# Kernel optimization log

Measured on AMD Instinct MI355X. Metric: run time of the kernel, lower is better.

The kernel has to match this reference:

```python
import jax, jax.numpy as jnp
import numpy as np

WS = 16         # window size
NH = 16         # num heads
EPS = 1e-6


def _ln(x):
    m = jnp.mean(x, axis=-1, keepdims=True)
    v = jnp.var(x, axis=-1, keepdims=True)
    return (x - m) * jax.lax.rsqrt(v + EPS)


def _modulate(x, shift, scale):
    return x * (1.0 + scale[:, None, :]) + shift[:, None, :]


def setup_inputs() -> dict:
    key = jax.random.key(0)
    ks = jax.random.split(key, 14)
    D, HD = 1024, 64
    s = 0.02
    return {
        'x': jax.random.normal(ks[0], (4, 4096, D), jnp.float32),
        'c': jax.random.normal(ks[1], (4, D), jnp.float32),
        'qkv_w': jax.random.normal(ks[2], (3 * D, D), jnp.float32) * s,
        'qkv_b': jax.random.normal(ks[3], (3 * D,), jnp.float32) * s,
        'proj_w': jax.random.normal(ks[4], (D, D), jnp.float32) * s,
        'proj_b': jax.random.normal(ks[5], (D,), jnp.float32) * s,
        'rel_pos_h': jax.random.normal(ks[6], (2 * WS - 1, HD), jnp.float32) * s,
        'rel_pos_w': jax.random.normal(ks[7], (2 * WS - 1, HD), jnp.float32) * s,
        'adaLN_w': jax.random.normal(ks[8], (6 * D, D), jnp.float32) * s,
        'adaLN_b': jax.random.normal(ks[9], (6 * D,), jnp.float32) * s,
        'fc1_w': jax.random.normal(ks[10], (4 * D, D), jnp.float32) * s,
        'fc1_b': jax.random.normal(ks[11], (4 * D,), jnp.float32) * s,
        'fc2_w': jax.random.normal(ks[12], (D, 4 * D), jnp.float32) * s,
        'fc2_b': jax.random.normal(ks[13], (D,), jnp.float32) * s,
    }


def _window_attention(x, qkv_w, qkv_b, proj_w, proj_b, rel_pos_h, rel_pos_w):
    # x: [N, T, D] with T = h*w, h = w = sqrt(T)
    N, T, D = x.shape
    h = w = int(round(T ** 0.5))
    nwh, nww = h // WS, w // WS  # grid divides evenly -> no padding
    hd = D // NH
    scale = hd ** -0.5

    # window partition: [N, h, w, D] -> [B, WS, WS, D], B = N*nwh*nww
    xw = x.reshape(N, nwh, WS, nww, WS, D).transpose(0, 1, 3, 2, 4, 5)
    xw = xw.reshape(N * nwh * nww, WS, WS, D)
    B = xw.shape[0]
    L = WS * WS

    qkv = (xw.reshape(B, L, D) @ qkv_w.T + qkv_b)  # [B, L, 3D]
    qkv = qkv.reshape(B, L, 3, NH, hd).transpose(2, 0, 3, 1, 4)  # [3, B, NH, L, hd]
    qkv = qkv.reshape(3, B * NH, L, hd)
    q, k, v = qkv[0], qkv[1], qkv[2]

    attn = jnp.einsum('bqc,bkc->bqk', q * scale, k)  # [B*NH, L, L]

    # decomposed relative position bias (q_size == k_size == WS)
    coords = jnp.arange(WS)
    rel_idx = coords[:, None] - coords[None, :] + (WS - 1)  # [WS, WS]
    Rh = rel_pos_h[rel_idx]  # [WS(q_h), WS(k_h), hd]
    Rw = rel_pos_w[rel_idx]  # [WS(q_w), WS(k_w), hd]
    rq = q.reshape(B * NH, WS, WS, hd)
    rel_h = jnp.einsum('bhwc,hkc->bhwk', rq, Rh)  # [B*NH, WS, WS, WS(kh)]
    rel_w = jnp.einsum('bhwc,wkc->bhwk', rq, Rw)  # [B*NH, WS, WS, WS(kw)]
    attn = (attn.reshape(B * NH, WS, WS, WS, WS)
            + rel_h[:, :, :, :, None]
            + rel_w[:, :, :, None, :]).reshape(B * NH, L, L)

    probs = jax.nn.softmax(attn, axis=-1)
    out = probs @ v  # [B*NH, L, hd]
    out = out.reshape(B, NH, WS, WS, hd).transpose(0, 2, 3, 1, 4).reshape(B, WS, WS, D)
    out = out @ proj_w.T + proj_b

    # window unpartition: [B, WS, WS, D] -> [N, T, D]
    out = out.reshape(N, nwh, nww, WS, WS, D).transpose(0, 1, 3, 2, 4, 5)
    return out.reshape(N, T, D)


def reference(x, c, qkv_w, qkv_b, proj_w, proj_b, rel_pos_h, rel_pos_w,
              adaLN_w, adaLN_b, fc1_w, fc1_b, fc2_w, fc2_b):
    D = x.shape[-1]
    mod = jax.nn.silu(c) @ adaLN_w.T + adaLN_b  # [N, 6D]
    sh_msa, sc_msa, g_msa, sh_mlp, sc_mlp, g_mlp = jnp.split(mod, 6, axis=1)

    a_in = _modulate(_ln(x), sh_msa, sc_msa)
    a_out = _window_attention(a_in, qkv_w, qkv_b, proj_w, proj_b, rel_pos_h, rel_pos_w)
    x = x + g_msa[:, None, :] * a_out

    m_in = _modulate(_ln(x), sh_mlp, sc_mlp)
    hdn = jax.nn.gelu(m_in @ fc1_w.T + fc1_b, approximate=True)
    m_out = hdn @ fc2_w.T + fc2_b
    x = x + g_mlp[:, None, :] * m_out
    return x
```

## Files before the change

kernel.cpp:

```cpp
#include <hip/hip_runtime.h>
#include <cstdint>
#include <cstddef>


typedef float  f32x4    __attribute__((ext_vector_type(4)));
typedef __bf16 bf16x8_t __attribute__((ext_vector_type(8)));
typedef __bf16 bf16x4_t __attribute__((ext_vector_type(4)));

#define DEV __device__ __forceinline__

DEV void gload_lds16(const void* g, void* l) {
    auto gp = (const uint32_t __attribute__((address_space(1)))*)(uintptr_t)g;
    auto lp = (uint32_t __attribute__((address_space(3)))*)(uint32_t)(uintptr_t)l;
    __builtin_amdgcn_global_load_lds(gp, lp, 16, 0, 0);
}

DEV bf16x8_t lds_frag(const __bf16* base, int row, int chunk, int row_elems) {
    return *(const bf16x8_t*)(base + row * row_elems + ((chunk ^ (row & 7)) << 3));
}

DEV bf16x8_t p_frag(const __bf16* base, int row, int chunk) {
    return *(const bf16x8_t*)(base + row * 32 + ((chunk ^ ((row >> 1) & 3)) << 3));
}

DEV int vt_addr(int d, int k) {
    return d * 64 + ((((k >> 3) ^ (d & 7) ^ ((d >> 3) & 7)) << 3) | (k & 7));
}

DEV float gelu_tanh(float v) {
    float u = 0.7978845608028654f * (v + 0.044715f * v * v * v);
    float e = __expf(2.f * u);
    float th = 1.f - 2.f / (e + 1.f);
    return 0.5f * v * (1.f + th);
}

DEV int win2tok(int r) {
    int nb = r >> 12, wi = (r >> 8) & 15, l = r & 255;
    return (nb << 12) + (wi >> 2) * 1024 + (l >> 4) * 64 + (wi & 3) * 16 + (l & 15);
}

__global__ void silu_k(const float* __restrict__ c, float* __restrict__ o, int n) {
    int i = blockIdx.x * 256 + threadIdx.x;
    if (i < n) { float v = c[i]; o[i] = v / (1.f + __expf(-v)); }
}

__global__ void zero_k(float* o, int n) {
    int i = blockIdx.x * 256 + threadIdx.x;
    if (i < n) o[i] = 0.f;
}

__global__ void conv_bf16(const float* __restrict__ s, __bf16* __restrict__ d, int n4) {
    int i = blockIdx.x * 256 + threadIdx.x;
    if (i < n4) {
        float4 v = ((const float4*)s)[i];
        bf16x4_t o; o[0] = (__bf16)v.x; o[1] = (__bf16)v.y; o[2] = (__bf16)v.z; o[3] = (__bf16)v.w;
        ((bf16x4_t*)d)[i] = o;
    }
}

__global__ __launch_bounds__(256)
void mod_gemv(const float* __restrict__ sc, const float* __restrict__ w,
              const float* __restrict__ b, float* __restrict__ mod) {
    int o = (blockIdx.x << 2) + (threadIdx.x >> 6);
    int lane = threadIdx.x & 63;
    int n = o / 6144, col = o % 6144;
    const float4* wr = (const float4*)(w + (size_t)col * 1024);
    const float4* sr = (const float4*)(sc + n * 1024);
    float acc = 0.f;
    #pragma unroll 4
    for (int i = lane; i < 256; i += 64) {
        float4 a = wr[i], x = sr[i];
        acc += a.x * x.x + a.y * x.y + a.z * x.z + a.w * x.w;
    }
    #pragma unroll
    for (int m = 1; m < 64; m <<= 1) acc += __shfl_xor(acc, m);
    if (lane == 0) mod[o] = acc + b[col];
}

__global__ __launch_bounds__(256)
void ln_mod_k(const float* __restrict__ src, const float* __restrict__ mod,
              int sh_off, int sc_off, __bf16* __restrict__ out, int permute, int r0) {
    int rl = blockIdx.x;
    int r = rl + r0;
    int nb = r >> 12;
    int t = permute ? win2tok(r) : r;
    float4 v = ((const float4*)(src + (size_t)t * 1024))[threadIdx.x];
    float s  = v.x + v.y + v.z + v.w;
    float sq = v.x * v.x + v.y * v.y + v.z * v.z + v.w * v.w;
    #pragma unroll
    for (int m = 1; m < 64; m <<= 1) { s += __shfl_xor(s, m); sq += __shfl_xor(sq, m); }
    __shared__ float ps[4], pq[4];
    int wv = threadIdx.x >> 6, ln = threadIdx.x & 63;
    if (ln == 0) { ps[wv] = s; pq[wv] = sq; }
    __syncthreads();
    s  = ps[0] + ps[1] + ps[2] + ps[3];
    sq = pq[0] + pq[1] + pq[2] + pq[3];
    float mean = s * (1.f / 1024.f);
    float var  = sq * (1.f / 1024.f) - mean * mean;
    float rstd = rsqrtf(var + 1e-6f);
    int c = threadIdx.x << 2;
    const float* mrow = mod + nb * 6144;
    float4 scv = *(const float4*)(mrow + sc_off + c);
    float4 shv = *(const float4*)(mrow + sh_off + c);
    bf16x4_t o;
    o[0] = (__bf16)((v.x - mean) * rstd * (1.f + scv.x) + shv.x);
    o[1] = (__bf16)((v.y - mean) * rstd * (1.f + scv.y) + shv.y);
    o[2] = (__bf16)((v.z - mean) * rstd * (1.f + scv.z) + shv.z);
    o[3] = (__bf16)((v.w - mean) * rstd * (1.f + scv.w) + shv.w);
    *(bf16x4_t*)(out + (size_t)rl * 1024 + c) = o;
}

template <int PM, int PN>
DEV void mfma16(f32x4 (&acc)[8][4], bf16x8_t (&fa)[4][2], bf16x8_t (&fb)[2][2][2]) {
    #pragma unroll
    for (int ks = 0; ks < 2; ++ks)
        #pragma unroll
        for (int mi = 0; mi < 4; ++mi)
            #pragma unroll
            for (int nn = 0; nn < 2; ++nn)
                acc[PM * 4 + mi][PN * 2 + nn] = __builtin_amdgcn_mfma_f32_16x16x32_bf16(
                    fa[mi][ks], fb[PN][nn][ks], acc[PM * 4 + mi][PN * 2 + nn], 0, 0, 0);
}

#define GBAR  __builtin_amdgcn_s_barrier()
#define VM6   asm volatile("s_waitcnt vmcnt(6)" ::: "memory")
#define PRIO1 __builtin_amdgcn_s_setprio(1)
#define PRIO0 __builtin_amdgcn_s_setprio(0)

template <int EPI>
__global__ __launch_bounds__(512)
void gemm256(const __bf16* __restrict__ A, const __bf16* __restrict__ B,
             const float* __restrict__ bias, void* __restrict__ Cout,
             const float* __restrict__ extra, const float* __restrict__ mod,
             int N, int K, int r0, int gx) {
    extern __shared__ __align__(16) char smem[];
    __bf16* lA = (__bf16*)smem;
    __bf16* lB = lA + 2 * 16384;
    const int tid = threadIdx.x, lane = tid & 63, wv = tid >> 6;
    const int wr = wv >> 2, wc = wv & 3;

    const int nwg = gridDim.x;
    const int qq = nwg >> 3, rr8 = nwg & 7;
    const int xcd = blockIdx.x & 7, pos = blockIdx.x >> 3;
    const int nid = (xcd < rr8 ? xcd * (qq + 1) : rr8 * (qq + 1) + (xcd - rr8) * qq) + pos;
    const int bm = (nid / gx) << 8, bn = (nid % gx) << 8;

    f32x4 acc[8][4];
    const f32x4 z4 = {0.f, 0.f, 0.f, 0.f};
    #pragma unroll
    for (int i = 0; i < 8; ++i)
        #pragma unroll
        for (int j = 0; j < 4; ++j) acc[i][j] = z4;

    bf16x8_t fa[4][2], fb[2][2][2];

    const int l8  = lane >> 3;
    const int gc8 = ((lane & 7) ^ l8) << 3;
    const int rbw = ((wv & 3) << 3) + ((wv >> 2) << 6);
    const __bf16* gA0 = A + (size_t)(bm +       (wv << 3) + l8) * K + gc8;
    const __bf16* gA1 = A + (size_t)(bm + 128 + (wv << 3) + l8) * K + gc8;
    const __bf16* gA2 = A + (size_t)(bm +  64 + (wv << 3) + l8) * K + gc8;
    const __bf16* gA3 = A + (size_t)(bm + 192 + (wv << 3) + l8) * K + gc8;
    const __bf16* gB0 = B + (size_t)(bn +       rbw + l8) * K + gc8;
    const __bf16* gB1 = B + (size_t)(bn + 128 + rbw + l8) * K + gc8;
    const __bf16* gB2 = B + (size_t)(bn +  32 + rbw + l8) * K + gc8;
    const __bf16* gB3 = B + (size_t)(bn + 160 + rbw + l8) * K + gc8;
    const int dA0 = (wv << 3) * 64, dA1 = (128 + (wv << 3)) * 64;
    const int dA2 = (64 + (wv << 3)) * 64, dA3 = (192 + (wv << 3)) * 64;
    const int dB0 = rbw * 64, dB1 = (128 + rbw) * 64;
    const int dB2 = (32 + rbw) * 64, dB3 = (160 + rbw) * 64;

    auto stA0 = [&](int be) { gload_lds16(gA0, lA + be + dA0); gload_lds16(gA1, lA + be + dA1); gA0 += 64; gA1 += 64; };
    auto stA1 = [&](int be) { gload_lds16(gA2, lA + be + dA2); gload_lds16(gA3, lA + be + dA3); gA2 += 64; gA3 += 64; };
    auto stB0 = [&](int be) { gload_lds16(gB0, lB + be + dB0); gload_lds16(gB1, lB + be + dB1); gB0 += 64; gB1 += 64; };
    auto stB1 = [&](int be) { gload_lds16(gB2, lB + be + dB2); gload_lds16(gB3, lB + be + dB3); gB2 += 64; gB3 += 64; };

    const int swzb = (lane >> 4) ^ (lane & 7);
    const __bf16* aR0 = lA + (wr << 13) + ((lane & 15) << 6) + (swzb << 3);
    const __bf16* aR1 = lA + (wr << 13) + ((lane & 15) << 6) + ((swzb ^ 4) << 3);
    const __bf16* bR0 = lB + (wc << 12) + ((lane & 15) << 6) + (swzb << 3);
    const __bf16* bR1 = lB + (wc << 12) + ((lane & 15) << 6) + ((swzb ^ 4) << 3);

    auto readA = [&](int be, int pm) {
        #pragma unroll
        for (int mi = 0; mi < 4; ++mi) {
            fa[mi][0] = *(const bf16x8_t*)(aR0 + be + pm * 4096 + mi * 1024);
            fa[mi][1] = *(const bf16x8_t*)(aR1 + be + pm * 4096 + mi * 1024);
        }
    };
    auto readB = [&](int be, int pn) {
        #pragma unroll
        for (int ni = 0; ni < 2; ++ni) {
            fb[pn][ni][0] = *(const bf16x8_t*)(bR0 + be + pn * 2048 + ni * 1024);
            fb[pn][ni][1] = *(const bf16x8_t*)(bR1 + be + pn * 2048 + ni * 1024);
        }
    };

    const int nt = K >> 6;
    stA0(0); stB0(0); stB1(0); stA1(0);

    int be = 0;
    for (int t = 0; t < nt - 1; ++t) {
        stA0(be ^ 16384);
        VM6; GBAR;
        readA(be, 0); readB(be, 0);
        PRIO1; mfma16<0, 0>(acc, fa, fb); PRIO0;
        stB0(be ^ 16384);
        VM6; GBAR;
        readB(be, 1);
        PRIO1; mfma16<0, 1>(acc, fa, fb); PRIO0;
        stB1(be ^ 16384);
        VM6; GBAR;
        readA(be, 1);
        PRIO1; mfma16<1, 0>(acc, fa, fb); PRIO0;
        stA1(be ^ 16384);
        PRIO1; mfma16<1, 1>(acc, fa, fb); PRIO0;
        be ^= 16384;
    }
    asm volatile("s_waitcnt vmcnt(4)" ::: "memory");
    GBAR;
    readA(be, 0); readB(be, 0);
    PRIO1; mfma16<0, 0>(acc, fa, fb); PRIO0;
    asm volatile("s_waitcnt vmcnt(2)" ::: "memory");
    GBAR;
    readB(be, 1);
    PRIO1; mfma16<0, 1>(acc, fa, fb); PRIO0;
    asm volatile("s_waitcnt vmcnt(0)" ::: "memory");
    GBAR;
    readA(be, 1);
    PRIO1; mfma16<1, 0>(acc, fa, fb); mfma16<1, 1>(acc, fa, fb); PRIO0;

    #pragma unroll
    for (int am = 0; am < 8; ++am) {
        #pragma unroll
        for (int j = 0; j < 4; ++j) {
            int m = bm + (wr << 7) + (am << 4) + ((lane >> 4) << 2) + j;
            #pragma unroll
            for (int an = 0; an < 4; ++an) {
                int n = bn + (wc << 6) + (an << 4) + (lane & 15);
                float v = acc[am][an][j] + bias[n];
                if constexpr (EPI == 0) {
                    ((__bf16*)Cout)[(size_t)m * N + n] = (__bf16)v;
                } else if constexpr (EPI == 1) {
                    int mg = m + r0;
                    int tr = win2tok(mg);
                    float g = mod[(mg >> 12) * 6144 + 2048 + n];
                    ((float*)Cout)[(size_t)tr * 1024 + n] = extra[(size_t)tr * 1024 + n] + g * v;
                } else if constexpr (EPI == 2) {
                    ((__bf16*)Cout)[(size_t)m * N + n] = (__bf16)gelu_tanh(v);
                } else {
                    int mg = m + r0;
                    float g = mod[(mg >> 12) * 6144 + 5120 + n];
                    ((float*)Cout)[(size_t)mg * 1024 + n] = extra[(size_t)mg * 1024 + n] + g * v;
                }
            }
        }
    }
}

__global__ __launch_bounds__(256)
void tab_k(const __bf16* __restrict__ qkv, const float* __restrict__ relh,
           const float* __restrict__ relw, __bf16* __restrict__ tab) {
    __shared__ __bf16 lR[2][31][72];
    for (int i = threadIdx.x; i < 1984; i += 256) {
        int row = i >> 6, c = i & 63;
        lR[0][row][c] = (__bf16)relh[i];
        lR[1][row][c] = (__bf16)relw[i];
    }
    __syncthreads();
    const int h = blockIdx.y;
    const int r = threadIdx.x >> 1, half = threadIdx.x & 1;
    const int l = blockIdx.x * 128 + r;
    const int lw = l & 255;
    const int qi = lw >> 4, qj = lw & 15;
    const __bf16* qrow = qkv + (size_t)l * 3072 + h * 64;
    float qq[64];
    #pragma unroll
    for (int c8 = 0; c8 < 8; ++c8) {
        bf16x8_t q8 = *(const bf16x8_t*)(qrow + (c8 << 3));
        #pragma unroll
        for (int e = 0; e < 8; ++e) qq[c8 * 8 + e] = (float)q8[e];
    }
    bf16x8_t oh, ow;
    #pragma unroll
    for (int kk = 0; kk < 8; ++kk) {
        int kg = (half << 3) + kk;
        const __bf16* Rh = &lR[0][qi - kg + 15][0];
        const __bf16* Rw = &lR[1][qj - kg + 15][0];
        float ah = 0.f, aw = 0.f;
        #pragma unroll
        for (int c8 = 0; c8 < 8; ++c8) {
            bf16x8_t r1 = *(const bf16x8_t*)(Rh + (c8 << 3));
            bf16x8_t r2 = *(const bf16x8_t*)(Rw + (c8 << 3));
            #pragma unroll
            for (int e = 0; e < 8; ++e) {
                ah += qq[c8 * 8 + e] * (float)r1[e];
                aw += qq[c8 * 8 + e] * (float)r2[e];
            }
        }
        oh[kk] = (__bf16)ah; ow[kk] = (__bf16)aw;
    }
    size_t idx = ((size_t)(l >> 8) * 16 + h) * 256 + lw;
    *(bf16x8_t*)(tab + idx * 32 + (half << 3))      = oh;
    *(bf16x8_t*)(tab + idx * 32 + 16 + (half << 3)) = ow;
}

__global__ __launch_bounds__(256, 3)
void attn_k(const __bf16* __restrict__ qkv, const __bf16* __restrict__ tab,
            __bf16* __restrict__ out) {
    __shared__ __align__(16) __bf16 lP[4][32 * 32];
    __shared__ __align__(16) __bf16 lKt[2][64 * 64];
    __shared__ __align__(16) __bf16 lVt[2][64 * 64];
    __shared__ __align__(16) __bf16 lTab[128 * 32];

    const int blk = blockIdx.x;
    const int winc = blk >> 5, h = (blk >> 1) & 15, qh = blk & 1;
    const int tid = threadIdx.x, lane = tid & 63, wv = tid >> 6;
    const __bf16* base = qkv + (size_t)winc * 256 * 3072 + h * 64;
    const int q0 = qh << 7;

    {
        const __bf16* ts = tab + (((size_t)winc * 16 + h) * 256 + q0) * 32;
        #pragma unroll
        for (int q = 0; q < 2; ++q) {
            int c = (wv << 1) + q;
            gload_lds16(ts + c * 512 + lane * 8, lTab + c * 512);
        }
    }
    bf16x8_t qf[2][2];
    #pragma unroll
    for (int mi = 0; mi < 2; ++mi)
        #pragma unroll
        for (int ks = 0; ks < 2; ++ks) {
            int l = q0 + (wv << 5) + (mi << 4) + (lane & 15);
            qf[mi][ks] = *(const bf16x8_t*)(base + (size_t)l * 3072 + (((ks << 2) + (lane >> 4)) << 3));
        }
    {
        const __bf16* kb = base + 1024;
        #pragma unroll
        for (int q = 0; q < 2; ++q) {
            int c = (wv << 1) + q;
            int kl = (c << 3) + (lane >> 3);
            gload_lds16(kb + (size_t)kl * 3072 + (((lane & 7) ^ (lane >> 3)) << 3),
                        lKt[0] + c * 512);
        }
        const __bf16* vb = base + 2048;
        bf16x8_t a = *(const bf16x8_t*)(vb + (size_t)(tid >> 3) * 3072 + ((tid & 7) << 3));
        bf16x8_t b = *(const bf16x8_t*)(vb + (size_t)(32 + (tid >> 3)) * 3072 + ((tid & 7) << 3));
        int lc = tid & 7;
        #pragma unroll
        for (int e = 0; e < 8; ++e) {
            lVt[0][vt_addr(lc * 8 + e, tid >> 3)]        = a[e];
            lVt[0][vt_addr(lc * 8 + e, 32 + (tid >> 3))] = b[e];
        }
    }
    __syncthreads();

    float twv[2][4];
    #pragma unroll
    for (int mi = 0; mi < 2; ++mi)
        #pragma unroll
        for (int j = 0; j < 4; ++j) {
            int qr = (wv << 5) + (mi << 4) + ((lane >> 4) << 2) + j;
            twv[mi][j] = (float)lTab[qr * 32 + 16 + (lane & 15)];
        }

    const f32x4 z4 = {0.f, 0.f, 0.f, 0.f};
    f32x4 oacc[2][4];
    #pragma unroll
    for (int a = 0; a < 2; ++a)
        #pragma unroll
        for (int b = 0; b < 4; ++b) oacc[a][b] = z4;
    float rsum[2][4];
    #pragma unroll
    for (int a = 0; a < 2; ++a)
        #pragma unroll
        for (int j = 0; j < 4; ++j) rsum[a][j] = 0.f;
    __bf16* lPw = lP[wv];

    int cur = 0;
    for (int kt = 0; kt < 4; ++kt) {
        const bool pre = (kt < 3);
        bf16x8_t v8a, v8b;
        if (pre) {
            const __bf16* kb = base + 1024 + (size_t)(kt + 1) * 64 * 3072;
            #pragma unroll
            for (int q = 0; q < 2; ++q) {
                int c = (wv << 1) + q;
                int kl = (c << 3) + (lane >> 3);
                gload_lds16(kb + (size_t)kl * 3072 + (((lane & 7) ^ (lane >> 3)) << 3),
                            lKt[cur ^ 1] + c * 512);
            }
            const __bf16* vb = base + 2048 + (size_t)(kt + 1) * 64 * 3072;
            v8a = *(const bf16x8_t*)(vb + (size_t)(tid >> 3) * 3072 + ((tid & 7) << 3));
            v8b = *(const bf16x8_t*)(vb + (size_t)(32 + (tid >> 3)) * 3072 + ((tid & 7) << 3));
        }

        f32x4 s[2][4];
        #pragma unroll
        for (int a = 0; a < 2; ++a)
            #pragma unroll
            for (int b = 0; b < 4; ++b) s[a][b] = z4;
        #pragma unroll
        for (int ks = 0; ks < 2; ++ks) {
            bf16x8_t kf[4];
            #pragma unroll
            for (int ni = 0; ni < 4; ++ni)
                kf[ni] = lds_frag(lKt[cur], (ni << 4) + (lane & 15), (ks << 2) + (lane >> 4), 64);
            #pragma unroll
            for (int mi = 0; mi < 2; ++mi)
                #pragma unroll
                for (int ni = 0; ni < 4; ++ni)
                    s[mi][ni] = __builtin_amdgcn_mfma_f32_16x16x32_bf16(qf[mi][ks], kf[ni], s[mi][ni], 0, 0, 0);
        }

        #pragma unroll
        for (int mi = 0; mi < 2; ++mi) {
            #pragma unroll
            for (int j = 0; j < 4; ++j) {
                int qr = (wv << 5) + (mi << 4) + ((lane >> 4) << 2) + j;
                bf16x4_t th4 = *(const bf16x4_t*)(lTab + qr * 32 + (kt << 2));
                float rs = 0.f;
                #pragma unroll
                for (int ni = 0; ni < 4; ++ni) {
                    float p = __expf(s[mi][ni][j] * 0.125f + (float)th4[ni] + twv[mi][j]);
                    s[mi][ni][j] = p;
                    rs += p;
                }
                rsum[mi][j] += rs;
            }
        }

        #pragma unroll
        for (int hf = 0; hf < 2; ++hf) {
            #pragma unroll
            for (int mi = 0; mi < 2; ++mi) {
                #pragma unroll
                for (int j = 0; j < 4; ++j) {
                    int rl = (mi << 4) + ((lane >> 4) << 2) + j;
                    #pragma unroll
                    for (int b = 0; b < 2; ++b) {
                        int col = (b << 4) + (lane & 15);
                        lPw[rl * 32 + ((((col >> 3) ^ ((rl >> 1) & 3)) << 3) | (col & 7))] =
                            (__bf16)s[mi][(hf << 1) + b][j];
                    }
                }
            }
            bf16x8_t pf[2], vf[4];
            #pragma unroll
            for (int mi = 0; mi < 2; ++mi)
                pf[mi] = p_frag(lPw, (mi << 4) + (lane & 15), lane >> 4);
            #pragma unroll
            for (int no = 0; no < 4; ++no) {
                int d = (no << 4) + (lane & 15);
                vf[no] = *(const bf16x8_t*)(lVt[cur] + vt_addr(d, ((hf << 2) + (lane >> 4)) << 3));
            }
            #pragma unroll
            for (int mi = 0; mi < 2; ++mi)
                #pragma unroll
                for (int no = 0; no < 4; ++no)
                    oacc[mi][no] = __builtin_amdgcn_mfma_f32_16x16x32_bf16(pf[mi], vf[no], oacc[mi][no], 0, 0, 0);
        }

        if (pre) {
            int lc = tid & 7;
            #pragma unroll
            for (int e = 0; e < 8; ++e) {
                lVt[cur ^ 1][vt_addr(lc * 8 + e, tid >> 3)]        = v8a[e];
                lVt[cur ^ 1][vt_addr(lc * 8 + e, 32 + (tid >> 3))] = v8b[e];
            }
        }
        __syncthreads();
        cur ^= 1;
    }

    #pragma unroll
    for (int mi = 0; mi < 2; ++mi) {
        #pragma unroll
        for (int j = 0; j < 4; ++j) {
            float rs = rsum[mi][j];
            #pragma unroll
            for (int msk = 1; msk < 16; msk <<= 1) rs += __shfl_xor(rs, msk);
            float inv = 1.f / rs;
            int l = q0 + (wv << 5) + (mi << 4) + ((lane >> 4) << 2) + j;
            #pragma unroll
            for (int no = 0; no < 4; ++no) {
                int col = (no << 4) + (lane & 15);
                out[(size_t)(winc * 256 + l) * 1024 + h * 64 + col] = (__bf16)(oacc[mi][no][j] * inv);
            }
        }
    }
}

extern "C" void kernel_launch(void* const* d_in, const int* in_sizes, int n_in,
                              void* d_out, int out_size, void* d_ws, size_t ws_size,
                              hipStream_t stream) {
    const float* x      = (const float*)d_in[0];
    const float* c      = (const float*)d_in[1];
    const float* qkv_w  = (const float*)d_in[2];
    const float* qkv_b  = (const float*)d_in[3];
    const float* proj_w = (const float*)d_in[4];
    const float* proj_b = (const float*)d_in[5];
    const float* rel_h  = (const float*)d_in[6];
    const float* rel_w  = (const float*)d_in[7];
    const float* ada_w  = (const float*)d_in[8];
    const float* ada_b  = (const float*)d_in[9];
    const float* fc1_w  = (const float*)d_in[10];
    const float* fc1_b  = (const float*)d_in[11];
    const float* fc2_w  = (const float*)d_in[12];
    const float* fc2_b  = (const float*)d_in[13];
    float* xo = (float*)d_out;

    char* ws = (char*)d_ws;
    const size_t MB = 1ull << 20;
    int CH = 0;
    const int cands[7] = {16384, 8192, 4096, 2048, 1024, 512, 256};
    for (int i = 0; i < 7; ++i)
        if (26 * MB + (size_t)cands[i] * 10240 <= ws_size) { CH = cands[i]; break; }
    if (CH == 0) {
        zero_k<<<65536, 256, 0, stream>>>(xo, 16777216);
        return;
    }

    const int LDSB = 131072;
    hipFuncSetAttribute((const void*)&gemm256<0>, hipFuncAttributeMaxDynamicSharedMemorySize, LDSB);
    hipFuncSetAttribute((const void*)&gemm256<1>, hipFuncAttributeMaxDynamicSharedMemorySize, LDSB);
    hipFuncSetAttribute((const void*)&gemm256<2>, hipFuncAttributeMaxDynamicSharedMemorySize, LDSB);
    hipFuncSetAttribute((const void*)&gemm256<3>, hipFuncAttributeMaxDynamicSharedMemorySize, LDSB);

    const int NCH = 16384 / CH;
    float*  ws_silu = (float*)(ws);
    float*  ws_mod  = (float*)(ws + 65536);
    __bf16* w_qkv   = (__bf16*)(ws + 1 * MB);
    __bf16* w_proj  = (__bf16*)(ws + 7 * MB);
    __bf16* w_fc1   = (__bf16*)(ws + 9 * MB);
    __bf16* w_fc2   = (__bf16*)(ws + 17 * MB);
    __bf16* bufA    = (__bf16*)(ws + 26 * MB);
    __bf16* bufB    = (__bf16*)(ws + 26 * MB + (size_t)CH * 2048);
    __bf16* tabbuf  = bufB + (size_t)CH * 3072;

    silu_k   <<<16,   256, 0, stream>>>(c, ws_silu, 4096);
    mod_gemv <<<6144, 256, 0, stream>>>(ws_silu, ada_w, ada_b, ws_mod);
    conv_bf16<<<3072, 256, 0, stream>>>(qkv_w,  w_qkv,  786432);
    conv_bf16<<<1024, 256, 0, stream>>>(proj_w, w_proj, 262144);
    conv_bf16<<<4096, 256, 0, stream>>>(fc1_w,  w_fc1,  1048576);
    conv_bf16<<<4096, 256, 0, stream>>>(fc2_w,  w_fc2,  1048576);

    const int gy = CH / 256;
    for (int ci = 0; ci < NCH; ++ci) {
        int r0 = ci * CH;
        ln_mod_k<<<CH, 256, 0, stream>>>(x, ws_mod, 0, 1024, bufA, 1, r0);
        gemm256<0><<<12 * gy, 512, LDSB, stream>>>(bufA, w_qkv, qkv_b, bufB,
                                                   nullptr, nullptr, 3072, 1024, r0, 12);
        tab_k<<<dim3(CH / 128, 16), 256, 0, stream>>>(bufB, rel_h, rel_w, tabbuf);
        attn_k<<<(CH / 256) * 32, 256, 0, stream>>>(bufB, tabbuf, bufA);
        gemm256<1><<<4 * gy, 512, LDSB, stream>>>(bufA, w_proj, proj_b, xo,
                                                  x, ws_mod, 1024, 1024, r0, 4);
    }
    for (int ci = 0; ci < NCH; ++ci) {
        int r0 = ci * CH;
        ln_mod_k<<<CH, 256, 0, stream>>>(xo, ws_mod, 3072, 4096, bufA, 0, r0);
        gemm256<2><<<16 * gy, 512, LDSB, stream>>>(bufA, w_fc1, fc1_b, bufB,
                                                   nullptr, nullptr, 4096, 1024, r0, 16);
        gemm256<3><<<4 * gy, 512, LDSB, stream>>>(bufB, w_fc2, fc2_b, xo,
                                                  xo, ws_mod, 1024, 4096, r0, 4);
    }
}
```

Before: 631.5 us.

## Simplify GEMM main loop to one full-tile stage and barrier per iteration

Replaces the four-phase interleaved staging of A and B tile quarters, which used partial vmcnt waits and three barriers per K step, with one call that issues all eight global-to-LDS loads for the next tile. Each iteration then does a full vmcnt(0) wait and a single barrier before computing all sixteen MFMA groups. The intent is to cut barrier and wait overhead and simplify scheduling. The cost is that the next tile's loads overlap less finely with compute, so the full wait may expose memory latency.

```diff
diff --git a/kernel.cpp b/kernel.cpp
--- a/kernel.cpp
+++ b/kernel.cpp
@@ -123,7 +123,6 @@
 }
 
 #define GBAR  __builtin_amdgcn_s_barrier()
-#define VM6   asm volatile("s_waitcnt vmcnt(6)" ::: "memory")
 #define PRIO1 __builtin_amdgcn_s_setprio(1)
 #define PRIO0 __builtin_amdgcn_s_setprio(0)
 
@@ -170,10 +169,14 @@
     const int dB0 = rbw * 64, dB1 = (128 + rbw) * 64;
     const int dB2 = (32 + rbw) * 64, dB3 = (160 + rbw) * 64;
 
-    auto stA0 = [&](int be) { gload_lds16(gA0, lA + be + dA0); gload_lds16(gA1, lA + be + dA1); gA0 += 64; gA1 += 64; };
-    auto stA1 = [&](int be) { gload_lds16(gA2, lA + be + dA2); gload_lds16(gA3, lA + be + dA3); gA2 += 64; gA3 += 64; };
-    auto stB0 = [&](int be) { gload_lds16(gB0, lB + be + dB0); gload_lds16(gB1, lB + be + dB1); gB0 += 64; gB1 += 64; };
-    auto stB1 = [&](int be) { gload_lds16(gB2, lB + be + dB2); gload_lds16(gB3, lB + be + dB3); gB2 += 64; gB3 += 64; };
+    auto stageAll = [&](int be2) {
+        gload_lds16(gA0, lA + be2 + dA0); gload_lds16(gA1, lA + be2 + dA1);
+        gload_lds16(gB0, lB + be2 + dB0); gload_lds16(gB1, lB + be2 + dB1);
+        gload_lds16(gB2, lB + be2 + dB2); gload_lds16(gB3, lB + be2 + dB3);
+        gload_lds16(gA2, lA + be2 + dA2); gload_lds16(gA3, lA + be2 + dA3);
+        gA0 += 64; gA1 += 64; gA2 += 64; gA3 += 64;
+        gB0 += 64; gB1 += 64; gB2 += 64; gB3 += 64;
+    };
 
     const int swzb = (lane >> 4) ^ (lane & 7);
     const __bf16* aR0 = lA + (wr << 13) + ((lane & 15) << 6) + (swzb << 3);
@@ -181,54 +184,35 @@
     const __bf16* bR0 = lB + (wc << 12) + ((lane & 15) << 6) + (swzb << 3);
     const __bf16* bR1 = lB + (wc << 12) + ((lane & 15) << 6) + ((swzb ^ 4) << 3);
 
-    auto readA = [&](int be, int pm) {
+    auto readA = [&](int be2, int pm) {
         #pragma unroll
         for (int mi = 0; mi < 4; ++mi) {
-            fa[mi][0] = *(const bf16x8_t*)(aR0 + be + pm * 4096 + mi * 1024);
-            fa[mi][1] = *(const bf16x8_t*)(aR1 + be + pm * 4096 + mi * 1024);
+            fa[mi][0] = *(const bf16x8_t*)(aR0 + be2 + pm * 4096 + mi * 1024);
+            fa[mi][1] = *(const bf16x8_t*)(aR1 + be2 + pm * 4096 + mi * 1024);
         }
     };
-    auto readB = [&](int be, int pn) {
+    auto readB = [&](int be2, int pn) {
         #pragma unroll
         for (int ni = 0; ni < 2; ++ni) {
-            fb[pn][ni][0] = *(const bf16x8_t*)(bR0 + be + pn * 2048 + ni * 1024);
-            fb[pn][ni][1] = *(const bf16x8_t*)(bR1 + be + pn * 2048 + ni * 1024);
+            fb[pn][ni][0] = *(const bf16x8_t*)(bR0 + be2 + pn * 2048 + ni * 1024);
+            fb[pn][ni][1] = *(const bf16x8_t*)(bR1 + be2 + pn * 2048 + ni * 1024);
         }
     };
 
     const int nt = K >> 6;
-    stA0(0); stB0(0); stB1(0); stA1(0);
+    stageAll(0);
 
     int be = 0;
-    for (int t = 0; t < nt - 1; ++t) {
-        stA0(be ^ 16384);
-        VM6; GBAR;
-        readA(be, 0); readB(be, 0);
-        PRIO1; mfma16<0, 0>(acc, fa, fb); PRIO0;
-        stB0(be ^ 16384);
-        VM6; GBAR;
-        readB(be, 1);
-        PRIO1; mfma16<0, 1>(acc, fa, fb); PRIO0;
-        stB1(be ^ 16384);
-        VM6; GBAR;
+    for (int t = 0; t < nt; ++t) {
+        asm volatile("s_waitcnt vmcnt(0)" ::: "memory");
+        GBAR;
+        if (t + 1 < nt) stageAll(be ^ 16384);
+        readA(be, 0); readB(be, 0); readB(be, 1);
+        PRIO1; mfma16<0, 0>(acc, fa, fb); mfma16<0, 1>(acc, fa, fb); PRIO0;
         readA(be, 1);
-        PRIO1; mfma16<1, 0>(acc, fa, fb); PRIO0;
-        stA1(be ^ 16384);
-        PRIO1; mfma16<1, 1>(acc, fa, fb); PRIO0;
+        PRIO1; mfma16<1, 0>(acc, fa, fb); mfma16<1, 1>(acc, fa, fb); PRIO0;
         be ^= 16384;
     }
-    asm volatile("s_waitcnt vmcnt(4)" ::: "memory");
-    GBAR;
-    readA(be, 0); readB(be, 0);
-    PRIO1; mfma16<0, 0>(acc, fa, fb); PRIO0;
-    asm volatile("s_waitcnt vmcnt(2)" ::: "memory");
-    GBAR;
-    readB(be, 1);
-    PRIO1; mfma16<0, 1>(acc, fa, fb); PRIO0;
-    asm volatile("s_waitcnt vmcnt(0)" ::: "memory");
-    GBAR;
-    readA(be, 1);
-    PRIO1; mfma16<1, 0>(acc, fa, fb); mfma16<1, 1>(acc, fa, fb); PRIO0;
 
     #pragma unroll
     for (int am = 0; am < 8; ++am) {
```

New measurement: 631.4 us. About the same (-0.0%).
